# Optimization experiments

Hardware: AMD Instinct MI355X
Metric: run time of the kernel (lower is better)

The kernel has to match this reference:

```python
import jax, jax.numpy as jnp
import numpy as np

N = 16384          # batch of signals
DIM_T = 256        # time steps per signal
DT = 0.01          # integration dt (intg_lev=1 -> dt_intg = dt)
NUF = 256          # num_units_feat
HID_XI = 128       # hidlayers_xi
HID_AUX = 64       # hidlayers_aux1_dec
LEN_INTG = DIM_T   # (dim_t-1)*intg_lev + 1 with intg_lev=1


def _linear_init(key, fan_in, fan_out):
    # torch nn.Linear default: U(-1/sqrt(fan_in), 1/sqrt(fan_in))
    s = 1.0 / np.sqrt(fan_in)
    kw, kb = jax.random.split(key)
    W = jax.random.uniform(kw, (fan_in, fan_out), minval=-s, maxval=s, dtype=jnp.float32)
    b = jax.random.uniform(kb, (fan_out,), minval=-s, maxval=s, dtype=jnp.float32)
    return W, b


def setup_inputs() -> dict:
    key = jax.random.key(0)
    ks = jax.random.split(key, 12)
    data = jax.random.normal(ks[0], (N, DIM_T), dtype=jnp.float32)
    omega = jax.random.normal(ks[1], (N, 1), dtype=jnp.float32)
    eps = jax.random.normal(ks[2], (N, 1), dtype=jnp.float32)
    # feature extractor (mlp branch): [dim_t+1 -> 256 -> 256], relu after both (actfun_output=True)
    W_feat1, b_feat1 = _linear_init(ks[3], DIM_T + 1, NUF)
    W_feat2, b_feat2 = _linear_init(ks[4], NUF, NUF)
    # xi mean head: MLP [256 -> 128 -> 1] then Softplus
    W_xim1, b_xim1 = _linear_init(ks[5], NUF, HID_XI)
    W_xim2, b_xim2 = _linear_init(ks[6], HID_XI, 1)
    # xi lnvar head: MLP [256 -> 128 -> 1]
    W_xil1, b_xil1 = _linear_init(ks[7], NUF, HID_XI)
    W_xil2, b_xil2 = _linear_init(ks[8], HID_XI, 1)
    # decoder aux1 MLP: [dim_z_aux1+1=2 -> 64 -> 1]
    W_aux1, b_aux1 = _linear_init(ks[9], 2, HID_AUX)
    W_aux2, b_aux2 = _linear_init(ks[10], HID_AUX, 1)
    return dict(data=data, omega=omega, eps=eps,
                W_feat1=W_feat1, b_feat1=b_feat1, W_feat2=W_feat2, b_feat2=b_feat2,
                W_xim1=W_xim1, b_xim1=b_xim1, W_xim2=W_xim2, b_xim2=b_xim2,
                W_xil1=W_xil1, b_xil1=b_xil1, W_xil2=W_xil2, b_xil2=b_xil2,
                W_aux1=W_aux1, b_aux1=b_aux1, W_aux2=W_aux2, b_aux2=b_aux2)


def reference(data, omega, eps,
              W_feat1, b_feat1, W_feat2, b_feat2,
              W_xim1, b_xim1, W_xim2, b_xim2,
              W_xil1, b_xil1, W_xil2, b_xil2,
              W_aux1, b_aux1, W_aux2, b_aux2):
    relu = jax.nn.relu
    # ---- encode_xi ----
    x_ = jnp.concatenate([data, omega], axis=1)                 # [n, dim_t+1]
    feat = relu(relu(x_ @ W_feat1 + b_feat1) @ W_feat2 + b_feat2)  # [n, 256]
    xi_mean = jax.nn.softplus(relu(feat @ W_xim1 + b_xim1) @ W_xim2 + b_xim2)  # [n, 1]
    xi_lnvar = relu(feat @ W_xil1 + b_xil1) @ W_xil2 + b_xil2                  # [n, 1]
    # ---- draw (reparameterization + clamp to feasible range [0, 1]) ----
    xi = xi_mean + jnp.exp(0.5 * xi_lnvar) * eps
    xi = jnp.clip(xi, 0.0, 1.0)
    # ---- decode: Euler odeint over LEN_INTG steps of state yy=[y, dy/dt] ----
    init_y = data[:, :1]                                        # [n, 1]
    initcond = jnp.concatenate([init_y, jnp.zeros_like(init_y)], axis=1)  # [n, 2]

    def step(yy, _):
        # physics: d[y, v]/dt = [v, 0]; aux MLP adds acceleration from (z_aux1=omega, y)
        aux_in = jnp.concatenate([omega, yy[:, :1]], axis=1)    # [n, 2]
        acc = relu(aux_in @ W_aux1 + b_aux1) @ W_aux2 + b_aux2  # [n, 1]
        dyy = jnp.concatenate([yy[:, 1:2], acc], axis=1)        # [n, 2]
        return yy + DT * dyy, yy

    _, yy_seq = jax.lax.scan(step, initcond, None, length=LEN_INTG)  # [len_intg, n, 2]
    y_seq = yy_seq[:, :, 0].T                                   # [n, dim_t] (intg_lev=1)
    t_intg = DT * jnp.arange(LEN_INTG, dtype=jnp.float32)       # [dim_t]
    x_PAB = jnp.exp(-jnp.abs(xi) * t_intg[None, :]) * y_seq     # [n, dim_t]
    return xi_mean, xi_lnvar, x_PAB
```

## Files before the change

### kernel.cpp

```cpp
#include <hip/hip_runtime.h>
#include <math.h>

#define NROWS 16384
#define DT_C 0.01f

typedef short s16x8 __attribute__((ext_vector_type(8)));
typedef float f32x4 __attribute__((ext_vector_type(4)));
typedef float f32x2 __attribute__((ext_vector_type(2)));

__device__ __forceinline__ unsigned short f2bf(float f) {
    unsigned u = __float_as_uint(f);
    u += 0x7fffu + ((u >> 16) & 1u);
    return (unsigned short)(u >> 16);
}
__device__ __forceinline__ unsigned pack2bf(float a, float b) {
    return (unsigned)f2bf(a) | ((unsigned)f2bf(b) << 16);
}
template <int CTRL>
__device__ __forceinline__ float dppadd(float v) {
    int x = __builtin_amdgcn_update_dpp(0, __float_as_int(v), CTRL, 0xF, 0xF, true);
    return v + __int_as_float(x);
}
__device__ __forceinline__ float sum8(float p) {
    p = dppadd<0xB1>(p);
    p = dppadd<0x4E>(p);
    p = dppadd<0x141>(p);
    return p;
}

__global__ __launch_bounds__(256) void prep_k(
    const float* __restrict__ Wf1, const float* __restrict__ Wf2,
    const float* __restrict__ Wm1, const float* __restrict__ Wl1,
    const float* __restrict__ bm1, const float* __restrict__ bl1,
    unsigned short* __restrict__ wpack, float* __restrict__ biasH)
{
    const int id = blockIdx.x * 256 + threadIdx.x;
    const int n  = id & 255;
    const int k8 = (id >> 8) & 31;
    const int s  = id >> 13;

    unsigned short tmp[8];
    #pragma unroll
    for (int j = 0; j < 8; ++j) {
        const int k = k8 * 8 + j;
        float v;
        if (s == 0)      v = Wf1[k * 256 + n];
        else if (s == 1) v = Wf2[k * 256 + n];
        else             v = (n < 128) ? Wm1[k * 128 + n] : Wl1[k * 128 + n - 128];
        tmp[j] = f2bf(v);
    }
    *(uint4*)&wpack[((s * 32 + k8) * 256 + n) * 8] = *(const uint4*)tmp;

    if (id < 256) biasH[id] = (id < 128) ? bm1[id] : bl1[id - 128];
}

__global__ __launch_bounds__(256, 2) void fused_k(
    const float* __restrict__ data, const float* __restrict__ omega,
    const float* __restrict__ eps_g,
    const unsigned short* __restrict__ wpack, const float* __restrict__ biasH,
    const float* __restrict__ bf1, const float* __restrict__ bf2,
    const float* __restrict__ w256g,
    const float* __restrict__ Wm2, const float* __restrict__ bm2,
    const float* __restrict__ Wl2, const float* __restrict__ bl2,
    const float* __restrict__ Wa1, const float* __restrict__ ba1,
    const float* __restrict__ Wa2, const float* __restrict__ ba2,
    float* __restrict__ out_mean, float* __restrict__ out_lnvar,
    float* __restrict__ xout)
{
    __shared__ __align__(16) unsigned char smem[33024];
    unsigned short* As1 = (unsigned short*)smem;
    unsigned short* Hs  = (unsigned short*)(smem + 16384);
    float* headsF = (float*)smem;
    float* omg = (float*)(smem + 32768);
    float* xiS = omg + 32;

    const int tid  = threadIdx.x;
    const int wid  = tid >> 6;
    const int lane = tid & 63;
    const int ln   = lane & 15;
    const int quad = lane >> 4;
    const int r0   = blockIdx.x * 32;

    {
        #pragma unroll
        for (int g2 = 0; g2 < 8; ++g2) {
            const int unit = g2 * 256 + tid;
            const int m    = unit >> 6;
            const int c16  = unit & 63;
            const int kblk = c16 >> 1;
            const int h    = c16 & 1;
            const float4 v = *(const float4*)&data[(size_t)(r0 + m) * 256 + c16 * 4];
            unsigned* d = (unsigned*)&As1[((kblk * 32) + (m ^ (kblk & 7))) * 8 + h * 4];
            d[0] = pack2bf(v.x, v.y);
            d[1] = pack2bf(v.z, v.w);
        }
        if (tid < 32) omg[tid] = omega[r0 + tid];
    }
    __syncthreads();

    {
        const int r   = tid >> 3;
        const int l   = tid & 7;
        const int row = r0 + r;
        const float om = omg[r];
        const float pseed = ba2[0] * 0.125f;

        f32x2 w1v[4], Av[4], w2v[4];
        #pragma unroll
        for (int i = 0; i < 4; ++i) {
            const f32x2 w0 = *(const f32x2*)&Wa1[l * 8 + i * 2];
            const f32x2 bb = *(const f32x2*)&ba1[l * 8 + i * 2];
            w1v[i] = *(const f32x2*)&Wa1[64 + l * 8 + i * 2];
            w2v[i] = *(const f32x2*)&Wa2[l * 8 + i * 2];
            Av[i]  = f32x2{fmaf(om, w0.x, bb.x), fmaf(om, w0.y, bb.y)};
        }

        auto partial = [&](float y) -> float {
            const f32x2 y2 = f32x2{y, y};
            f32x2 acc2 = f32x2{pseed, 0.f};
            #pragma unroll
            for (int i = 0; i < 4; ++i) {
                f32x2 h = __builtin_elementwise_fma(y2, w1v[i], Av[i]);
                h = __builtin_elementwise_max(h, f32x2{0.f, 0.f});
                acc2 = __builtin_elementwise_fma(h, w2v[i], acc2);
            }
            return acc2.x + acc2.y;
        };

        const float y0 = data[(size_t)row * 256];
        float ym = y0;
        float yc = y0;
        const float DT2 = DT_C * DT_C;
        float pr = sum8(partial(ym));

        float* orow = xout + (size_t)row * 256 + l * 4;
        for (int tb = 0; tb < 8; ++tb) {
            float cur[4];
            #pragma unroll
            for (int j = 0; j < 32; ++j) {
                if ((j >> 2) == l) cur[j & 3] = ym;
                float pn = sum8(partial(yc));
                const float ynext = fmaf(DT2, pr, fmaf(2.f, yc, -ym));
                ym = yc; yc = ynext; pr = pn;
            }
            *(float4*)&orow[tb * 32] = *(const float4*)cur;
        }
    }

    f32x4 acc[2][4];

    auto seed = [&](const float* bias) {
        #pragma unroll
        for (int nt = 0; nt < 4; ++nt) {
            const float b = bias[wid * 64 + nt * 16 + ln];
            acc[0][nt] = f32x4{b, b, b, b};
            acc[1][nt] = acc[0][nt];
        }
    };

    auto run_stage = [&](const unsigned short* Ap, const unsigned short* wp) {
        #pragma unroll
        for (int c = 0; c < 4; ++c) {
            #pragma unroll
            for (int kk = 0; kk < 2; ++kk) {
                const int kb   = kk * 4 + quad;
                const int kblk = c * 8 + kb;
                const int f    = kblk & 7;
                s16x8 b0 = *(const s16x8*)&wp[((size_t)(kblk * 256) + wid * 64 + 0 * 16 + ln) * 8];
                s16x8 b1 = *(const s16x8*)&wp[((size_t)(kblk * 256) + wid * 64 + 1 * 16 + ln) * 8];
                s16x8 b2 = *(const s16x8*)&wp[((size_t)(kblk * 256) + wid * 64 + 2 * 16 + ln) * 8];
                s16x8 b3 = *(const s16x8*)&wp[((size_t)(kblk * 256) + wid * 64 + 3 * 16 + ln) * 8];
                s16x8 a0 = *(const s16x8*)&Ap[(kblk * 32 + (ln ^ f)) * 8];
                s16x8 a1 = *(const s16x8*)&Ap[(kblk * 32 + ((ln ^ f) + 16)) * 8];
                acc[0][0] = __builtin_amdgcn_mfma_f32_16x16x32_bf16(a0, b0, acc[0][0], 0, 0, 0);
                acc[1][0] = __builtin_amdgcn_mfma_f32_16x16x32_bf16(a1, b0, acc[1][0], 0, 0, 0);
                acc[0][1] = __builtin_amdgcn_mfma_f32_16x16x32_bf16(a0, b1, acc[0][1], 0, 0, 0);
                acc[1][1] = __builtin_amdgcn_mfma_f32_16x16x32_bf16(a1, b1, acc[1][1], 0, 0, 0);
                acc[0][2] = __builtin_amdgcn_mfma_f32_16x16x32_bf16(a0, b2, acc[0][2], 0, 0, 0);
                acc[1][2] = __builtin_amdgcn_mfma_f32_16x16x32_bf16(a1, b2, acc[1][2], 0, 0, 0);
                acc[0][3] = __builtin_amdgcn_mfma_f32_16x16x32_bf16(a0, b3, acc[0][3], 0, 0, 0);
                acc[1][3] = __builtin_amdgcn_mfma_f32_16x16x32_bf16(a1, b3, acc[1][3], 0, 0, 0);
            }
        }
    };

    auto write_packed = [&](unsigned short* dst, bool addOm) {
        #pragma unroll
        for (int nt = 0; nt < 4; ++nt) {
            const int col = wid * 64 + nt * 16 + ln;
            const int kg  = col >> 3, f = kg & 7, jj = col & 7;
            const float wo = addOm ? w256g[col] : 0.f;
            #pragma unroll
            for (int mt = 0; mt < 2; ++mt) {
                #pragma unroll
                for (int r = 0; r < 4; ++r) {
                    const int row = mt * 16 + quad * 4 + r;
                    float v = acc[mt][nt][r];
                    if (addOm) v = fmaf(omg[row], wo, v);
                    v = fmaxf(v, 0.f);
                    dst[(kg * 32 + (row ^ f)) * 8 + jj] = f2bf(v);
                }
            }
        }
    };

    seed(bf1);
    run_stage(As1, wpack);
    write_packed(Hs, true);
    __syncthreads();
    seed(bf2);
    run_stage(Hs, wpack + 65536);
    write_packed(As1, false);
    __syncthreads();
    seed(biasH);
    run_stage(As1, wpack + 131072);
    __syncthreads();
    #pragma unroll
    for (int nt = 0; nt < 4; ++nt) {
        const int col = wid * 64 + nt * 16 + ln;
        #pragma unroll
        for (int mt = 0; mt < 2; ++mt) {
            #pragma unroll
            for (int r = 0; r < 4; ++r) {
                const int row = mt * 16 + quad * 4 + r;
                headsF[row * 256 + ((col + row * 8) & 255)] = fmaxf(acc[mt][nt][r], 0.f);
            }
        }
    }
    __syncthreads();

    {
        const int m = tid >> 3, l = tid & 7;
        float pm = 0.f, pl = 0.f;
        #pragma unroll
        for (int q = 0; q < 4; ++q) {
            const int c0 = l * 16 + q * 4;
            const float4 hm = *(const float4*)&headsF[m * 256 + ((c0 + m * 8) & 255)];
            const float4 wm = *(const float4*)&Wm2[c0];
            const float4 hl = *(const float4*)&headsF[m * 256 + ((128 + c0 + m * 8) & 255)];
            const float4 wl = *(const float4*)&Wl2[c0];
            pm = fmaf(hm.w, wm.w, fmaf(hm.z, wm.z, fmaf(hm.y, wm.y, fmaf(hm.x, wm.x, pm))));
            pl = fmaf(hl.w, wl.w, fmaf(hl.z, wl.z, fmaf(hl.y, wl.y, fmaf(hl.x, wl.x, pl))));
        }
        pm = sum8(pm);
        pl = sum8(pl);
        if (l == 0) {
            const float xm  = pm + bm2[0];
            const float mean = fmaxf(xm, 0.f) + log1pf(expf(-fabsf(xm)));
            const float lnv  = pl + bl2[0];
            out_mean[r0 + m]  = mean;
            out_lnvar[r0 + m] = lnv;
            float xi = mean + expf(0.5f * lnv) * eps_g[r0 + m];
            xiS[m] = fminf(fmaxf(xi, 0.f), 1.f);
        }
    }
    __syncthreads();

    {
        const int r   = tid >> 3;
        const int l   = tid & 7;
        const float nxdt = -xiS[r] * DT_C;
        float* orow = xout + (size_t)(r0 + r) * 256 + l * 4;
        #pragma unroll
        for (int tb = 0; tb < 8; ++tb) {
            float4 v = *(const float4*)&orow[tb * 32];
            const int c0 = tb * 32 + l * 4;
            v.x *= __expf(nxdt * (float)(c0 + 0));
            v.y *= __expf(nxdt * (float)(c0 + 1));
            v.z *= __expf(nxdt * (float)(c0 + 2));
            v.w *= __expf(nxdt * (float)(c0 + 3));
            *(float4*)&orow[tb * 32] = v;
        }
    }
}

extern "C" void kernel_launch(void* const* d_in, const int* in_sizes, int n_in,
                              void* d_out, int out_size, void* d_ws, size_t ws_size,
                              hipStream_t stream)
{
    const float* data    = (const float*)d_in[0];
    const float* omega   = (const float*)d_in[1];
    const float* eps     = (const float*)d_in[2];
    const float* W_feat1 = (const float*)d_in[3];
    const float* b_feat1 = (const float*)d_in[4];
    const float* W_feat2 = (const float*)d_in[5];
    const float* b_feat2 = (const float*)d_in[6];
    const float* W_xim1  = (const float*)d_in[7];
    const float* b_xim1  = (const float*)d_in[8];
    const float* W_xim2  = (const float*)d_in[9];
    const float* b_xim2  = (const float*)d_in[10];
    const float* W_xil1  = (const float*)d_in[11];
    const float* b_xil1  = (const float*)d_in[12];
    const float* W_xil2  = (const float*)d_in[13];
    const float* b_xil2  = (const float*)d_in[14];
    const float* W_aux1  = (const float*)d_in[15];
    const float* b_aux1  = (const float*)d_in[16];
    const float* W_aux2  = (const float*)d_in[17];
    const float* b_aux2  = (const float*)d_in[18];

    float* out_mean  = (float*)d_out;
    float* out_lnvar = out_mean + NROWS;
    float* out_x     = out_lnvar + NROWS;

    unsigned short* wpack = (unsigned short*)d_ws;
    float* biasH = (float*)((char*)d_ws + 3 * 32 * 256 * 8 * 2);

    prep_k<<<96, 256, 0, stream>>>(W_feat1, W_feat2, W_xim1, W_xil1,
                                   b_xim1, b_xil1, wpack, biasH);
    fused_k<<<512, 256, 0, stream>>>(data, omega, eps, wpack, biasH,
                                     b_feat1, b_feat2, W_feat1 + 256 * 256,
                                     W_xim2, b_xim2, W_xil2, b_xil2,
                                     W_aux1, b_aux1, W_aux2, b_aux2,
                                     out_mean, out_lnvar, out_x);
}
```

Measured before the change: 141.1 us.

## Move ODE integration after xi computation and fuse decay scaling into it

The Euler ODE loop moves to after the MLP/xi stage, so the exponential decay factor is applied directly when each output value is produced. This removes the separate read-modify-write pass over the output and its per-element exp calls. The loop is also restructured to advance two steps per iteration, evaluating two aux-MLP partials with their DPP reductions together to expose more instruction-level parallelism. In exchange, the decay is built as a running product of exp(-xi*dt), which can drift numerically, and the serial ODE now starts only after the matmul stages finish, so it no longer overlaps with them.

```diff
diff --git a/kernel.cpp b/kernel.cpp
--- a/kernel.cpp
+++ b/kernel.cpp
@@ -98,55 +98,6 @@
     }
     __syncthreads();
 
-    {
-        const int r   = tid >> 3;
-        const int l   = tid & 7;
-        const int row = r0 + r;
-        const float om = omg[r];
-        const float pseed = ba2[0] * 0.125f;
-
-        f32x2 w1v[4], Av[4], w2v[4];
-        #pragma unroll
-        for (int i = 0; i < 4; ++i) {
-            const f32x2 w0 = *(const f32x2*)&Wa1[l * 8 + i * 2];
-            const f32x2 bb = *(const f32x2*)&ba1[l * 8 + i * 2];
-            w1v[i] = *(const f32x2*)&Wa1[64 + l * 8 + i * 2];
-            w2v[i] = *(const f32x2*)&Wa2[l * 8 + i * 2];
-            Av[i]  = f32x2{fmaf(om, w0.x, bb.x), fmaf(om, w0.y, bb.y)};
-        }
-
-        auto partial = [&](float y) -> float {
-            const f32x2 y2 = f32x2{y, y};
-            f32x2 acc2 = f32x2{pseed, 0.f};
-            #pragma unroll
-            for (int i = 0; i < 4; ++i) {
-                f32x2 h = __builtin_elementwise_fma(y2, w1v[i], Av[i]);
-                h = __builtin_elementwise_max(h, f32x2{0.f, 0.f});
-                acc2 = __builtin_elementwise_fma(h, w2v[i], acc2);
-            }
-            return acc2.x + acc2.y;
-        };
-
-        const float y0 = data[(size_t)row * 256];
-        float ym = y0;
-        float yc = y0;
-        const float DT2 = DT_C * DT_C;
-        float pr = sum8(partial(ym));
-
-        float* orow = xout + (size_t)row * 256 + l * 4;
-        for (int tb = 0; tb < 8; ++tb) {
-            float cur[4];
-            #pragma unroll
-            for (int j = 0; j < 32; ++j) {
-                if ((j >> 2) == l) cur[j & 3] = ym;
-                float pn = sum8(partial(yc));
-                const float ynext = fmaf(DT2, pr, fmaf(2.f, yc, -ym));
-                ym = yc; yc = ynext; pr = pn;
-            }
-            *(float4*)&orow[tb * 32] = *(const float4*)cur;
-        }
-    }
-
     f32x4 acc[2][4];
 
     auto seed = [&](const float* bias) {
@@ -259,17 +210,61 @@
     {
         const int r   = tid >> 3;
         const int l   = tid & 7;
-        const float nxdt = -xiS[r] * DT_C;
-        float* orow = xout + (size_t)(r0 + r) * 256 + l * 4;
-        #pragma unroll
+        const int row = r0 + r;
+        const float om = omg[r];
+        const float pseed = ba2[0] * 0.125f;
+
+        f32x2 w1v[4], Av[4], w2v[4];
+        #pragma unroll
+        for (int i = 0; i < 4; ++i) {
+            const f32x2 w0 = *(const f32x2*)&Wa1[l * 8 + i * 2];
+            const f32x2 bb = *(const f32x2*)&ba1[l * 8 + i * 2];
+            w1v[i] = *(const f32x2*)&Wa1[64 + l * 8 + i * 2];
+            w2v[i] = *(const f32x2*)&Wa2[l * 8 + i * 2];
+            Av[i]  = f32x2{fmaf(om, w0.x, bb.x), fmaf(om, w0.y, bb.y)};
+        }
+
+        auto partial = [&](float y) -> float {
+            const f32x2 y2 = f32x2{y, y};
+            f32x2 acc2 = f32x2{pseed, 0.f};
+            #pragma unroll
+            for (int i = 0; i < 4; ++i) {
+                f32x2 h = __builtin_elementwise_fma(y2, w1v[i], Av[i]);
+                h = __builtin_elementwise_max(h, f32x2{0.f, 0.f});
+                acc2 = __builtin_elementwise_fma(h, w2v[i], acc2);
+            }
+            return acc2.x + acc2.y;
+        };
+
+        const float xi   = xiS[r];
+        const float dfac = expf(-xi * DT_C);
+        const float df2  = dfac * dfac;
+        const float y0   = data[(size_t)row * 256];
+        const float DT2  = DT_C * DT_C;
+
+        float u  = y0;
+        float v  = y0;
+        float au = sum8(partial(u));
+        float du = 1.f;
+
+        float* orow = xout + (size_t)row * 256 + l * 4;
         for (int tb = 0; tb < 8; ++tb) {
-            float4 v = *(const float4*)&orow[tb * 32];
-            const int c0 = tb * 32 + l * 4;
-            v.x *= __expf(nxdt * (float)(c0 + 0));
-            v.y *= __expf(nxdt * (float)(c0 + 1));
-            v.z *= __expf(nxdt * (float)(c0 + 2));
-            v.w *= __expf(nxdt * (float)(c0 + 3));
-            *(float4*)&orow[tb * 32] = v;
+            float cur[4];
+            #pragma unroll
+            for (int p = 0; p < 16; ++p) {
+                const int j0 = 2 * p;
+                if ((j0 >> 2) == l) cur[j0 & 3] = u * du;
+                const float w = fmaf(DT2, au, fmaf(2.f, v, -u));
+                if (((j0 + 1) >> 2) == l) cur[(j0 + 1) & 3] = v * (du * dfac);
+                float av_ = partial(v);
+                float aw_ = partial(w);
+                av_ = sum8(av_);
+                aw_ = sum8(aw_);
+                const float x = fmaf(DT2, av_, fmaf(2.f, w, -v));
+                u = w; v = x; au = aw_;
+                du *= df2;
+            }
+            *(float4*)&orow[tb * 32] = *(const float4*)cur;
         }
     }
 }
```

Result: no change. 140.4 us (-0.5%).

## Move ODE scan after MLP, fuse decay, and double rows per block

Applied to the files above, without the earlier changes.

Each block now handles 64 rows with 512 threads. The MFMA tiles are reshaped so each wave covers 4 row tiles by 2 column tiles. The Euler ODE recurrence moves after the xi computation, and the exp(-xi t) decay is applied inline through a running multiplicative factor. This removes the second read-modify-write pass over the output. The ODE work is split 4 lanes per row instead of 8, with half the threads idle during that phase. The repeated-product decay may drift slightly from the direct exp, and the larger LDS footprint may reduce occupancy.

```diff
diff --git a/kernel.cpp b/kernel.cpp
--- a/kernel.cpp
+++ b/kernel.cpp
@@ -20,6 +20,11 @@
 __device__ __forceinline__ float dppadd(float v) {
     int x = __builtin_amdgcn_update_dpp(0, __float_as_int(v), CTRL, 0xF, 0xF, true);
     return v + __int_as_float(x);
+}
+__device__ __forceinline__ float sum4(float p) {
+    p = dppadd<0xB1>(p);
+    p = dppadd<0x4E>(p);
+    return p;
 }
 __device__ __forceinline__ float sum8(float p) {
     p = dppadd<0xB1>(p);
@@ -54,7 +59,7 @@
     if (id < 256) biasH[id] = (id < 128) ? bm1[id] : bl1[id - 128];
 }
 
-__global__ __launch_bounds__(256, 2) void fused_k(
+__global__ __launch_bounds__(512, 2) void fused_k(
     const float* __restrict__ data, const float* __restrict__ omega,
     const float* __restrict__ eps_g,
     const unsigned short* __restrict__ wpack, const float* __restrict__ biasH,
@@ -67,94 +72,45 @@
     float* __restrict__ out_mean, float* __restrict__ out_lnvar,
     float* __restrict__ xout)
 {
-    __shared__ __align__(16) unsigned char smem[33024];
+    __shared__ __align__(16) unsigned char smem[66048];
     unsigned short* As1 = (unsigned short*)smem;
-    unsigned short* Hs  = (unsigned short*)(smem + 16384);
+    unsigned short* Hs  = (unsigned short*)(smem + 32768);
     float* headsF = (float*)smem;
-    float* omg = (float*)(smem + 32768);
-    float* xiS = omg + 32;
+    float* omg = (float*)(smem + 65536);
+    float* xiS = (float*)(smem + 65792);
 
     const int tid  = threadIdx.x;
     const int wid  = tid >> 6;
     const int lane = tid & 63;
     const int ln   = lane & 15;
     const int quad = lane >> 4;
-    const int r0   = blockIdx.x * 32;
+    const int r0   = blockIdx.x * 64;
 
     {
         #pragma unroll
         for (int g2 = 0; g2 < 8; ++g2) {
-            const int unit = g2 * 256 + tid;
+            const int unit = g2 * 512 + tid;
             const int m    = unit >> 6;
             const int c16  = unit & 63;
             const int kblk = c16 >> 1;
             const int h    = c16 & 1;
             const float4 v = *(const float4*)&data[(size_t)(r0 + m) * 256 + c16 * 4];
-            unsigned* d = (unsigned*)&As1[((kblk * 32) + (m ^ (kblk & 7))) * 8 + h * 4];
+            unsigned* d = (unsigned*)&As1[((kblk * 64) + (m ^ (kblk & 7))) * 8 + h * 4];
             d[0] = pack2bf(v.x, v.y);
             d[1] = pack2bf(v.z, v.w);
         }
-        if (tid < 32) omg[tid] = omega[r0 + tid];
-    }
-    __syncthreads();
-
-    {
-        const int r   = tid >> 3;
-        const int l   = tid & 7;
-        const int row = r0 + r;
-        const float om = omg[r];
-        const float pseed = ba2[0] * 0.125f;
-
-        f32x2 w1v[4], Av[4], w2v[4];
-        #pragma unroll
-        for (int i = 0; i < 4; ++i) {
-            const f32x2 w0 = *(const f32x2*)&Wa1[l * 8 + i * 2];
-            const f32x2 bb = *(const f32x2*)&ba1[l * 8 + i * 2];
-            w1v[i] = *(const f32x2*)&Wa1[64 + l * 8 + i * 2];
-            w2v[i] = *(const f32x2*)&Wa2[l * 8 + i * 2];
-            Av[i]  = f32x2{fmaf(om, w0.x, bb.x), fmaf(om, w0.y, bb.y)};
-        }
-
-        auto partial = [&](float y) -> float {
-            const f32x2 y2 = f32x2{y, y};
-            f32x2 acc2 = f32x2{pseed, 0.f};
-            #pragma unroll
-            for (int i = 0; i < 4; ++i) {
-                f32x2 h = __builtin_elementwise_fma(y2, w1v[i], Av[i]);
-                h = __builtin_elementwise_max(h, f32x2{0.f, 0.f});
-                acc2 = __builtin_elementwise_fma(h, w2v[i], acc2);
-            }
-            return acc2.x + acc2.y;
-        };
-
-        const float y0 = data[(size_t)row * 256];
-        float ym = y0;
-        float yc = y0;
-        const float DT2 = DT_C * DT_C;
-        float pr = sum8(partial(ym));
-
-        float* orow = xout + (size_t)row * 256 + l * 4;
-        for (int tb = 0; tb < 8; ++tb) {
-            float cur[4];
-            #pragma unroll
-            for (int j = 0; j < 32; ++j) {
-                if ((j >> 2) == l) cur[j & 3] = ym;
-                float pn = sum8(partial(yc));
-                const float ynext = fmaf(DT2, pr, fmaf(2.f, yc, -ym));
-                ym = yc; yc = ynext; pr = pn;
-            }
-            *(float4*)&orow[tb * 32] = *(const float4*)cur;
-        }
-    }
-
-    f32x4 acc[2][4];
+        if (tid < 64) omg[tid] = omega[r0 + tid];
+    }
+    __syncthreads();
+
+    f32x4 acc[4][2];
 
     auto seed = [&](const float* bias) {
         #pragma unroll
-        for (int nt = 0; nt < 4; ++nt) {
-            const float b = bias[wid * 64 + nt * 16 + ln];
-            acc[0][nt] = f32x4{b, b, b, b};
-            acc[1][nt] = acc[0][nt];
+        for (int nt = 0; nt < 2; ++nt) {
+            const float b = bias[wid * 32 + nt * 16 + ln];
+            #pragma unroll
+            for (int mt = 0; mt < 4; ++mt) acc[mt][nt] = f32x4{b, b, b, b};
         }
     };
 
@@ -166,39 +122,33 @@
                 const int kb   = kk * 4 + quad;
                 const int kblk = c * 8 + kb;
                 const int f    = kblk & 7;
-                s16x8 b0 = *(const s16x8*)&wp[((size_t)(kblk * 256) + wid * 64 + 0 * 16 + ln) * 8];
-                s16x8 b1 = *(const s16x8*)&wp[((size_t)(kblk * 256) + wid * 64 + 1 * 16 + ln) * 8];
-                s16x8 b2 = *(const s16x8*)&wp[((size_t)(kblk * 256) + wid * 64 + 2 * 16 + ln) * 8];
-                s16x8 b3 = *(const s16x8*)&wp[((size_t)(kblk * 256) + wid * 64 + 3 * 16 + ln) * 8];
-                s16x8 a0 = *(const s16x8*)&Ap[(kblk * 32 + (ln ^ f)) * 8];
-                s16x8 a1 = *(const s16x8*)&Ap[(kblk * 32 + ((ln ^ f) + 16)) * 8];
-                acc[0][0] = __builtin_amdgcn_mfma_f32_16x16x32_bf16(a0, b0, acc[0][0], 0, 0, 0);
-                acc[1][0] = __builtin_amdgcn_mfma_f32_16x16x32_bf16(a1, b0, acc[1][0], 0, 0, 0);
-                acc[0][1] = __builtin_amdgcn_mfma_f32_16x16x32_bf16(a0, b1, acc[0][1], 0, 0, 0);
-                acc[1][1] = __builtin_amdgcn_mfma_f32_16x16x32_bf16(a1, b1, acc[1][1], 0, 0, 0);
-                acc[0][2] = __builtin_amdgcn_mfma_f32_16x16x32_bf16(a0, b2, acc[0][2], 0, 0, 0);
-                acc[1][2] = __builtin_amdgcn_mfma_f32_16x16x32_bf16(a1, b2, acc[1][2], 0, 0, 0);
-                acc[0][3] = __builtin_amdgcn_mfma_f32_16x16x32_bf16(a0, b3, acc[0][3], 0, 0, 0);
-                acc[1][3] = __builtin_amdgcn_mfma_f32_16x16x32_bf16(a1, b3, acc[1][3], 0, 0, 0);
+                s16x8 b0 = *(const s16x8*)&wp[((size_t)(kblk * 256) + wid * 32 + 0 * 16 + ln) * 8];
+                s16x8 b1 = *(const s16x8*)&wp[((size_t)(kblk * 256) + wid * 32 + 1 * 16 + ln) * 8];
+                #pragma unroll
+                for (int mt = 0; mt < 4; ++mt) {
+                    s16x8 a = *(const s16x8*)&Ap[((size_t)kblk * 64 + ((ln ^ f) + 16 * mt)) * 8];
+                    acc[mt][0] = __builtin_amdgcn_mfma_f32_16x16x32_bf16(a, b0, acc[mt][0], 0, 0, 0);
+                    acc[mt][1] = __builtin_amdgcn_mfma_f32_16x16x32_bf16(a, b1, acc[mt][1], 0, 0, 0);
+                }
             }
         }
     };
 
     auto write_packed = [&](unsigned short* dst, bool addOm) {
         #pragma unroll
-        for (int nt = 0; nt < 4; ++nt) {
-            const int col = wid * 64 + nt * 16 + ln;
+        for (int nt = 0; nt < 2; ++nt) {
+            const int col = wid * 32 + nt * 16 + ln;
             const int kg  = col >> 3, f = kg & 7, jj = col & 7;
             const float wo = addOm ? w256g[col] : 0.f;
             #pragma unroll
-            for (int mt = 0; mt < 2; ++mt) {
+            for (int mt = 0; mt < 4; ++mt) {
                 #pragma unroll
                 for (int r = 0; r < 4; ++r) {
                     const int row = mt * 16 + quad * 4 + r;
                     float v = acc[mt][nt][r];
                     if (addOm) v = fmaf(omg[row], wo, v);
                     v = fmaxf(v, 0.f);
-                    dst[(kg * 32 + (row ^ f)) * 8 + jj] = f2bf(v);
+                    dst[(kg * 64 + (row ^ f)) * 8 + jj] = f2bf(v);
                 }
             }
         }
@@ -216,10 +166,10 @@
     run_stage(As1, wpack + 131072);
     __syncthreads();
     #pragma unroll
-    for (int nt = 0; nt < 4; ++nt) {
-        const int col = wid * 64 + nt * 16 + ln;
-        #pragma unroll
-        for (int mt = 0; mt < 2; ++mt) {
+    for (int nt = 0; nt < 2; ++nt) {
+        const int col = wid * 32 + nt * 16 + ln;
+        #pragma unroll
+        for (int mt = 0; mt < 4; ++mt) {
             #pragma unroll
             for (int r = 0; r < 4; ++r) {
                 const int row = mt * 16 + quad * 4 + r;
@@ -256,20 +206,65 @@
     }
     __syncthreads();
 
+    if (tid >= 256) return;
+
     {
-        const int r   = tid >> 3;
-        const int l   = tid & 7;
-        const float nxdt = -xiS[r] * DT_C;
-        float* orow = xout + (size_t)(r0 + r) * 256 + l * 4;
-        #pragma unroll
-        for (int tb = 0; tb < 8; ++tb) {
-            float4 v = *(const float4*)&orow[tb * 32];
-            const int c0 = tb * 32 + l * 4;
-            v.x *= __expf(nxdt * (float)(c0 + 0));
-            v.y *= __expf(nxdt * (float)(c0 + 1));
-            v.z *= __expf(nxdt * (float)(c0 + 2));
-            v.w *= __expf(nxdt * (float)(c0 + 3));
-            *(float4*)&orow[tb * 32] = v;
+        const int r   = tid >> 2;
+        const int l   = tid & 3;
+        const int row = r0 + r;
+        const float om = omg[r];
+        const float pseed = ba2[0] * 0.25f;
+
+        f32x2 w1v[8], Av[8], w2v[8];
+        #pragma unroll
+        for (int i = 0; i < 8; ++i) {
+            const f32x2 w0 = *(const f32x2*)&Wa1[l * 16 + i * 2];
+            const f32x2 bb = *(const f32x2*)&ba1[l * 16 + i * 2];
+            w1v[i] = *(const f32x2*)&Wa1[64 + l * 16 + i * 2];
+            w2v[i] = *(const f32x2*)&Wa2[l * 16 + i * 2];
+            Av[i]  = f32x2{fmaf(om, w0.x, bb.x), fmaf(om, w0.y, bb.y)};
+        }
+
+        auto partial = [&](float y) -> float {
+            const f32x2 y2 = f32x2{y, y};
+            f32x2 aA = f32x2{pseed, 0.f};
+            f32x2 aB = f32x2{0.f, 0.f};
+            #pragma unroll
+            for (int i = 0; i < 4; ++i) {
+                f32x2 h = __builtin_elementwise_fma(y2, w1v[i], Av[i]);
+                h = __builtin_elementwise_max(h, f32x2{0.f, 0.f});
+                aA = __builtin_elementwise_fma(h, w2v[i], aA);
+            }
+            #pragma unroll
+            for (int i = 4; i < 8; ++i) {
+                f32x2 g = __builtin_elementwise_fma(y2, w1v[i], Av[i]);
+                g = __builtin_elementwise_max(g, f32x2{0.f, 0.f});
+                aB = __builtin_elementwise_fma(g, w2v[i], aB);
+            }
+            return (aA.x + aA.y) + (aB.x + aB.y);
+        };
+
+        const float xi   = xiS[r];
+        const float dfac = expf(-xi * DT_C);
+        const float y0   = data[(size_t)row * 256];
+        float ym = y0;
+        float yc = y0;
+        float d  = 1.f;
+        const float DT2 = DT_C * DT_C;
+        float pr = sum4(partial(ym));
+
+        float* orow = xout + (size_t)row * 256 + l * 4;
+        for (int tb = 0; tb < 16; ++tb) {
+            float cur[4];
+            #pragma unroll
+            for (int j = 0; j < 16; ++j) {
+                if ((j >> 2) == l) cur[j & 3] = ym * d;
+                float pn = sum4(partial(yc));
+                const float ynext = fmaf(DT2, pr, fmaf(2.f, yc, -ym));
+                ym = yc; yc = ynext; pr = pn;
+                d *= dfac;
+            }
+            *(float4*)&orow[tb * 16] = *(const float4*)cur;
         }
     }
 }
@@ -307,7 +302,7 @@
 
     prep_k<<<96, 256, 0, stream>>>(W_feat1, W_feat2, W_xim1, W_xil1,
                                    b_xim1, b_xil1, wpack, biasH);
-    fused_k<<<512, 256, 0, stream>>>(data, omega, eps, wpack, biasH,
+    fused_k<<<256, 512, 0, stream>>>(data, omega, eps, wpack, biasH,
                                      b_feat1, b_feat2, W_feat1 + 256 * 256,
                                      W_xim2, b_xim2, W_xil2, b_xil2,
                                      W_aux1, b_aux1, W_aux2, b_aux2,
```

New measurement: 137.4 us (median of 2 runs). 1.03x faster.
